# Performance work log

Hardware: AMD Instinct MI355X
Metric: run time of the kernel (lower is better)

Reference implementation:

```python
import jax, jax.numpy as jnp
import numpy as np

NEG_SLOPE = 0.2  # PyG GATConv default leaky_relu slope

def _xavier(key, shape):
    fan_in, fan_out = shape[0], shape[-1]
    lim = float(np.sqrt(6.0 / (fan_in + fan_out)))
    return jax.random.uniform(key, shape, jnp.float32, -lim, lim)

def setup_inputs() -> dict:
    key = jax.random.key(0)
    ks = jax.random.split(key, 12)
    B, N, F_in, Hd, H = 32768, 12, 128, 64, 4
    return {
        'node_features': jax.random.normal(ks[0], (B, N, F_in), jnp.float32),
        # GAT layer 1: 128 -> 64 per head, 4 heads, concat
        'W1': _xavier(ks[1], (F_in, H * Hd)),
        'att_src1': _xavier(ks[2], (H, Hd)),
        'att_dst1': _xavier(ks[3], (H, Hd)),
        'b1': jnp.zeros((H * Hd,), jnp.float32),
        # GAT layer 2: 256 -> 64, 1 head, no concat
        'W2': _xavier(ks[4], (H * Hd, Hd)),
        'att_src2': _xavier(ks[5], (1, Hd)),
        'att_dst2': _xavier(ks[6], (1, Hd)),
        'b2': jnp.zeros((Hd,), jnp.float32),
        # classifier 64 -> 32 -> 1
        'Wc1': _xavier(ks[7], (Hd, Hd // 2)),
        'bc1': jnp.zeros((Hd // 2,), jnp.float32),
        'Wc2': _xavier(ks[8], (Hd // 2, 1)),
        'bc2': jnp.zeros((1,), jnp.float32),
    }

def gat_layer(x, W, a_src, a_dst, b, concat):
    # x: [B, N, Fin]; fully-connected graph with self loops (PyG add_self_loops=True)
    B, N, _ = x.shape
    H, D = a_src.shape
    h = (x @ W).reshape(B, N, H, D)                      # [B,N,H,D]
    es = jnp.einsum('bnhd,hd->bhn', h, a_src)            # source logits per node
    ed = jnp.einsum('bnhd,hd->bhn', h, a_dst)            # dest logits per node
    # logits[b,h,i,j] for edge j->i
    logits = jax.nn.leaky_relu(ed[:, :, :, None] + es[:, :, None, :], NEG_SLOPE)
    alpha = jax.nn.softmax(logits, axis=-1)              # softmax over sources j
    out = jnp.einsum('bhij,bjhd->bihd', alpha, h)        # [B,N,H,D]
    if concat:
        out = out.reshape(B, N, H * D)
    else:
        out = out.mean(axis=2)
    return out + b

def reference(node_features, W1, att_src1, att_dst1, b1, W2, att_src2, att_dst2, b2, Wc1, bc1, Wc2, bc2):
    x = gat_layer(node_features, W1, att_src1, att_dst1, b1, concat=True)
    x = jax.nn.elu(x)
    x = gat_layer(x, W2, att_src2, att_dst2, b2, concat=False)
    x = jax.nn.elu(x)
    g = x.mean(axis=1)                                   # global mean pool over 12 nodes
    hcls = jax.nn.relu(g @ Wc1 + bc1)
    return hcls @ Wc2 + bc2                              # [B, 1]
```

## Files before the change

kernel.cpp:

```cpp
#include <hip/hip_runtime.h>
#include <math.h>


typedef __attribute__((ext_vector_type(8))) short bf16x8;
typedef __attribute__((ext_vector_type(4))) float f32x4;
typedef unsigned short u16;
typedef unsigned int u32;

constexpr int NN  = 12;
constexpr int FIN = 128;
constexpr int C1  = 256;
constexpr int DD  = 64;
#define NEG 0.2f

constexpr int WS_W1H = 0, WS_W1L = 32768, WS_W2H = 65536, WS_W2L = 81920;

__device__ __forceinline__ u16 f2bf(float f) {
    u32 u = __float_as_uint(f);
    u += 0x7fffu + ((u >> 16) & 1u);
    return (u16)(u >> 16);
}
__device__ __forceinline__ float bf2f(u16 h) { return __uint_as_float(((u32)h) << 16); }
__device__ __forceinline__ float bflo(u32 u) { return __uint_as_float(u << 16); }
__device__ __forceinline__ float bfhi(u32 u) { return __uint_as_float(u & 0xffff0000u); }

__global__ void prep_weights(const float* __restrict__ W1,
                             const float* __restrict__ W2,
                             u16* __restrict__ ws) {
    int idx = blockIdx.x * 256 + threadIdx.x;
    if (idx < 32768) {
        int j = idx & 7, lane = (idx >> 3) & 63, ks = (idx >> 9) & 3, nt = idx >> 11;
        int k = ks * 32 + (lane >> 4) * 8 + j;
        int c = nt * 16 + (lane & 15);
        float v = W1[k * C1 + c];
        u16 hi = f2bf(v);
        ws[WS_W1H + idx] = hi;
        ws[WS_W1L + idx] = f2bf(v - bf2f(hi));
    } else if (idx < 49152) {
        int i2 = idx - 32768;
        int j = i2 & 7, lane = (i2 >> 3) & 63, ks = (i2 >> 9) & 7, nt = i2 >> 12;
        int k = ks * 32 + (lane >> 4) * 8 + j;
        int c = nt * 16 + (lane & 15);
        float v = W2[k * DD + c];
        u16 hi = f2bf(v);
        ws[WS_W2H + i2] = hi;
        ws[WS_W2L + i2] = f2bf(v - bf2f(hi));
    }
}

__global__ __launch_bounds__(256, 3) void gat_fused(
    const float* __restrict__ x_in,
    const u16*  __restrict__ wtab,
    const float* __restrict__ asrc1, const float* __restrict__ adst1,
    const float* __restrict__ b1,
    const float* __restrict__ asrc2, const float* __restrict__ adst2,
    const float* __restrict__ b2,
    const float* __restrict__ Wc1,  const float* __restrict__ bc1,
    const float* __restrict__ Wc2,  const float* __restrict__ bc2,
    float* __restrict__ out)
{
    __shared__ __align__(16) unsigned char s_union[34816];
    u16* s_xh  = (u16*)s_union;
    u16* s_xl  = s_xh + 32 * 136;
    u16* s_h1h = (u16*)s_union;
    u16* s_h1l = s_h1h + 32 * 264;
    __shared__ __align__(16) float s_alpha[2][4][NN][NN];
    __shared__ float s_es[2][4][NN], s_ed[2][4][NN];
    __shared__ __align__(16) float s_alpha2[2][NN][NN];
    __shared__ float s_es2[2][NN], s_ed2[2][NN];
    __shared__ __align__(16) float s_h2[24 * DD];
    __shared__ float s_gmean[2][DD];
    __shared__ float s_hc[2][32];

    const int t = threadIdx.x;
    const int lane = t & 63, wave = t >> 6;
    const long b0 = (long)blockIdx.x * 2;

    {
        const float4* src = (const float4*)(x_in + b0 * NN * FIN);
        #pragma unroll
        for (int j = 0; j < 3; ++j) {
            int p = j * 256 + t;
            float4 v = src[p];
            int row = p >> 5, col = (p & 31) * 4;
            ushort4 h, l;
            h.x = f2bf(v.x); l.x = f2bf(v.x - bf2f(h.x));
            h.y = f2bf(v.y); l.y = f2bf(v.y - bf2f(h.y));
            h.z = f2bf(v.z); l.z = f2bf(v.z - bf2f(h.z));
            h.w = f2bf(v.w); l.w = f2bf(v.w - bf2f(h.w));
            *(ushort4*)&s_xh[row * 136 + col] = h;
            *(ushort4*)&s_xl[row * 136 + col] = l;
        }
        for (int i = t; i < 544; i += 256) {
            ((u32*)(s_xh + 24 * 136))[i] = 0u;
            ((u32*)(s_xl + 24 * 136))[i] = 0u;
        }
    }
    __syncthreads();

    {
        const int arow = lane & 15, aks = lane >> 4;
        bf16x8 ah[2][4], al[2][4];
        #pragma unroll
        for (int m = 0; m < 2; ++m)
            #pragma unroll
            for (int ks = 0; ks < 4; ++ks) {
                int off = (m * 16 + arow) * 136 + ks * 32 + aks * 8;
                ah[m][ks] = *(const bf16x8*)&s_xh[off];
                al[m][ks] = *(const bf16x8*)&s_xl[off];
            }
        __syncthreads();

        #pragma unroll
        for (int nti = 0; nti < 4; ++nti) {
            const int nt = wave * 4 + nti;
            bf16x8 bh[4], bl[4];
            #pragma unroll
            for (int ks = 0; ks < 4; ++ks) {
                int off = ((nt * 4 + ks) * 64 + lane) * 8;
                bh[ks] = *(const bf16x8*)&wtab[WS_W1H + off];
                bl[ks] = *(const bf16x8*)&wtab[WS_W1L + off];
            }
            f32x4 acc[2] = { {0.f,0.f,0.f,0.f}, {0.f,0.f,0.f,0.f} };
            #pragma unroll
            for (int ks = 0; ks < 4; ++ks)
                #pragma unroll
                for (int m = 0; m < 2; ++m) {
                    acc[m] = __builtin_amdgcn_mfma_f32_16x16x32_bf16(ah[m][ks], bh[ks], acc[m], 0, 0, 0);
                    acc[m] = __builtin_amdgcn_mfma_f32_16x16x32_bf16(ah[m][ks], bl[ks], acc[m], 0, 0, 0);
                    acc[m] = __builtin_amdgcn_mfma_f32_16x16x32_bf16(al[m][ks], bh[ks], acc[m], 0, 0, 0);
                    acc[m] = __builtin_amdgcn_mfma_f32_16x16x32_bf16(al[m][ks], bl[ks], acc[m], 0, 0, 0);
                }
            const int ccol = nt * 16 + (lane & 15);
            #pragma unroll
            for (int m = 0; m < 2; ++m)
                #pragma unroll
                for (int r = 0; r < 4; ++r) {
                    int row = m * 16 + (lane >> 4) * 4 + r;
                    float v = acc[m][r];
                    u16 hi = f2bf(v);
                    s_h1h[row * 264 + ccol] = hi;
                    s_h1l[row * 264 + ccol] = f2bf(v - bf2f(hi));
                }
        }
    }
    __syncthreads();

    if (t < 192) {
        int tmp = t;
        const int n = tmp % NN; tmp /= NN;
        const int h = tmp & 3; tmp >>= 2;
        const int sflag = tmp & 1;
        const int g = tmp >> 1;
        const float* att = (sflag ? adst1 : asrc1) + h * DD;
        const int base = (g * NN + n) * 264 + h * DD;
        float sum = 0.f;
        #pragma unroll
        for (int it = 0; it < 8; ++it) {
            const int ch = ((it + t) & 7) * 8;
            uint4 uh = *(const uint4*)&s_h1h[base + ch];
            uint4 ul = *(const uint4*)&s_h1l[base + ch];
            float4 a0 = *(const float4*)&att[ch];
            float4 a1 = *(const float4*)&att[ch + 4];
            sum += (bflo(uh.x) + bflo(ul.x)) * a0.x;
            sum += (bfhi(uh.x) + bfhi(ul.x)) * a0.y;
            sum += (bflo(uh.y) + bflo(ul.y)) * a0.z;
            sum += (bfhi(uh.y) + bfhi(ul.y)) * a0.w;
            sum += (bflo(uh.z) + bflo(ul.z)) * a1.x;
            sum += (bfhi(uh.z) + bfhi(ul.z)) * a1.y;
            sum += (bflo(uh.w) + bflo(ul.w)) * a1.z;
            sum += (bfhi(uh.w) + bfhi(ul.w)) * a1.w;
        }
        if (sflag) s_ed[g][h][n] = sum; else s_es[g][h][n] = sum;
    }
    __syncthreads();

    if (t < 96) {
        const int i = t % NN;
        const int h = (t / NN) & 3;
        const int g = t / (NN * 4);
        const float edv = s_ed[g][h][i];
        float l[NN];
        float m = -3.4e38f;
        #pragma unroll
        for (int j = 0; j < NN; ++j) {
            float v = edv + s_es[g][h][j];
            v = (v >= 0.f) ? v : NEG * v;
            l[j] = v; m = fmaxf(m, v);
        }
        float s = 0.f;
        #pragma unroll
        for (int j = 0; j < NN; ++j) { float p = __expf(l[j] - m); l[j] = p; s += p; }
        const float inv = 1.f / s;
        #pragma unroll
        for (int j = 0; j < NN; ++j) s_alpha[g][h][i][j] = l[j] * inv;
    }
    __syncthreads();

    {
        const int c = t;
        const int hh = c >> 6;
        const float bias = b1[c];
        #pragma unroll
        for (int g = 0; g < 2; ++g) {
            float hcol[NN];
            #pragma unroll
            for (int j = 0; j < NN; ++j) {
                int off = (g * NN + j) * 264 + c;
                hcol[j] = bf2f(s_h1h[off]) + bf2f(s_h1l[off]);
            }
            float x2v[NN];
            #pragma unroll
            for (int i = 0; i < NN; ++i) {
                const float4* ar = (const float4*)&s_alpha[g][hh][i][0];
                float4 q0 = ar[0], q1 = ar[1], q2 = ar[2];
                float o = q0.x*hcol[0] + q0.y*hcol[1] + q0.z*hcol[2] + q0.w*hcol[3]
                        + q1.x*hcol[4] + q1.y*hcol[5] + q1.z*hcol[6] + q1.w*hcol[7]
                        + q2.x*hcol[8] + q2.y*hcol[9] + q2.z*hcol[10] + q2.w*hcol[11];
                o += bias;
                x2v[i] = (o > 0.f) ? o : (__expf(o) - 1.f);
            }
            #pragma unroll
            for (int i = 0; i < NN; ++i) {
                int off = (g * NN + i) * 264 + c;
                u16 hi = f2bf(x2v[i]);
                s_h1h[off] = hi;
                s_h1l[off] = f2bf(x2v[i] - bf2f(hi));
            }
        }
    }
    __syncthreads();

    {
        const int arow = lane & 15, aks = lane >> 4;
        f32x4 acc[2] = { {0.f,0.f,0.f,0.f}, {0.f,0.f,0.f,0.f} };
        #pragma unroll
        for (int ks = 0; ks < 8; ++ks) {
            int woff = ((wave * 8 + ks) * 64 + lane) * 8;
            bf16x8 bh = *(const bf16x8*)&wtab[WS_W2H + woff];
            bf16x8 bl = *(const bf16x8*)&wtab[WS_W2L + woff];
            #pragma unroll
            for (int m = 0; m < 2; ++m) {
                int off = (m * 16 + arow) * 264 + ks * 32 + aks * 8;
                bf16x8 ah = *(const bf16x8*)&s_h1h[off];
                bf16x8 al = *(const bf16x8*)&s_h1l[off];
                acc[m] = __builtin_amdgcn_mfma_f32_16x16x32_bf16(ah, bh, acc[m], 0, 0, 0);
                acc[m] = __builtin_amdgcn_mfma_f32_16x16x32_bf16(ah, bl, acc[m], 0, 0, 0);
                acc[m] = __builtin_amdgcn_mfma_f32_16x16x32_bf16(al, bh, acc[m], 0, 0, 0);
                acc[m] = __builtin_amdgcn_mfma_f32_16x16x32_bf16(al, bl, acc[m], 0, 0, 0);
            }
        }
        const int ccol = wave * 16 + (lane & 15);
        #pragma unroll
        for (int m = 0; m < 2; ++m)
            #pragma unroll
            for (int r = 0; r < 4; ++r) {
                int row = m * 16 + (lane >> 4) * 4 + r;
                if (row < 24) s_h2[row * DD + ccol] = acc[m][r];
            }
    }
    __syncthreads();

    if (t < 48) {
        const int n = t % NN;
        const int sflag = (t / NN) & 1;
        const int g = t / (NN * 2);
        const float* att = sflag ? adst2 : asrc2;
        const float* row = s_h2 + (g * NN + n) * DD;
        float sum = 0.f;
        #pragma unroll
        for (int it = 0; it < 16; ++it) {
            const int dch = ((it + t) & 15) * 4;
            float4 hv = *(const float4*)&row[dch];
            float4 av = *(const float4*)&att[dch];
            sum += hv.x * av.x + hv.y * av.y + hv.z * av.z + hv.w * av.w;
        }
        if (sflag) s_ed2[g][n] = sum; else s_es2[g][n] = sum;
    }
    __syncthreads();
    if (t < 24) {
        const int i = t % NN;
        const int g = t / NN;
        const float edv = s_ed2[g][i];
        float l[NN];
        float m = -3.4e38f;
        #pragma unroll
        for (int j = 0; j < NN; ++j) {
            float v = edv + s_es2[g][j];
            v = (v >= 0.f) ? v : NEG * v;
            l[j] = v; m = fmaxf(m, v);
        }
        float s = 0.f;
        #pragma unroll
        for (int j = 0; j < NN; ++j) { float p = __expf(l[j] - m); l[j] = p; s += p; }
        const float inv = 1.f / s;
        #pragma unroll
        for (int j = 0; j < NN; ++j) s_alpha2[g][i][j] = l[j] * inv;
    }
    __syncthreads();

    if (t < 128) {
        const int g = t >> 6;
        const int d = t & 63;
        float hcol[NN];
        #pragma unroll
        for (int j = 0; j < NN; ++j) hcol[j] = s_h2[(g * NN + j) * DD + d];
        const float bias = b2[d];
        float gsum = 0.f;
        #pragma unroll
        for (int i = 0; i < NN; ++i) {
            const float4* ar = (const float4*)&s_alpha2[g][i][0];
            float4 q0 = ar[0], q1 = ar[1], q2 = ar[2];
            float o = q0.x*hcol[0] + q0.y*hcol[1] + q0.z*hcol[2] + q0.w*hcol[3]
                    + q1.x*hcol[4] + q1.y*hcol[5] + q1.z*hcol[6] + q1.w*hcol[7]
                    + q2.x*hcol[8] + q2.y*hcol[9] + q2.z*hcol[10] + q2.w*hcol[11];
            o += bias;
            o = (o > 0.f) ? o : (__expf(o) - 1.f);
            gsum += o;
        }
        s_gmean[g][d] = gsum * (1.f / 12.f);
    }
    __syncthreads();

    if (t < 64) {
        const int g = t >> 5;
        const int m = t & 31;
        float sum = bc1[m];
        #pragma unroll
        for (int d = 0; d < DD; ++d) sum = fmaf(s_gmean[g][d], Wc1[d * 32 + m], sum);
        s_hc[g][m] = (sum > 0.f) ? sum : 0.f;
    }
    __syncthreads();
    if (t < 2) {
        float sum = bc2[0];
        #pragma unroll
        for (int m = 0; m < 32; ++m) sum = fmaf(s_hc[t][m], Wc2[m], sum);
        out[b0 + t] = sum;
    }
}

extern "C" void kernel_launch(void* const* d_in, const int* in_sizes, int n_in,
                              void* d_out, int out_size, void* d_ws, size_t ws_size,
                              hipStream_t stream) {
    const float* x     = (const float*)d_in[0];
    const float* W1    = (const float*)d_in[1];
    const float* asrc1 = (const float*)d_in[2];
    const float* adst1 = (const float*)d_in[3];
    const float* b1    = (const float*)d_in[4];
    const float* W2    = (const float*)d_in[5];
    const float* asrc2 = (const float*)d_in[6];
    const float* adst2 = (const float*)d_in[7];
    const float* b2    = (const float*)d_in[8];
    const float* Wc1   = (const float*)d_in[9];
    const float* bc1   = (const float*)d_in[10];
    const float* Wc2   = (const float*)d_in[11];
    const float* bc2   = (const float*)d_in[12];
    float* outp = (float*)d_out;

    const int B = in_sizes[0] / (NN * FIN);
    u16* wtab = (u16*)d_ws;

    hipLaunchKernelGGL(prep_weights, dim3(192), dim3(256), 0, stream, W1, W2, wtab);
    hipLaunchKernelGGL(gat_fused, dim3(B / 2), dim3(256), 0, stream,
                       x, wtab, asrc1, adst1, b1, asrc2, adst2, b2,
                       Wc1, bc1, Wc2, bc2, outp);
}
```

Baseline: 628.8 us.

## Swizzle MFMA operand layout, keep h1 in fp32, drop lo*lo MFMA term

Stores the split-bf16 A operands (x and the layer-2 input) in LDS using an XOR-swizzled, fragment-major layout so each lane reads one contiguous 16-byte chunk without bank conflicts. The layer-1 output h1 is now kept as fp32 in padded LDS rows instead of being split into hi/lo bf16 halves, which removes the conversion and decode work. The lo*lo MFMA term is dropped in both GEMMs, removing a quarter of the matrix instructions at a small accuracy cost. The s_h2 rows are padded to 68 to reduce bank conflicts, and an extra barrier is added so the layer-2 input can reuse the h1 buffer.

```diff
diff --git a/kernel.cpp b/kernel.cpp
--- a/kernel.cpp
+++ b/kernel.cpp
@@ -21,8 +21,7 @@
     return (u16)(u >> 16);
 }
 __device__ __forceinline__ float bf2f(u16 h) { return __uint_as_float(((u32)h) << 16); }
-__device__ __forceinline__ float bflo(u32 u) { return __uint_as_float(u << 16); }
-__device__ __forceinline__ float bfhi(u32 u) { return __uint_as_float(u & 0xffff0000u); }
+__device__ __forceinline__ int swz(int u) { return u ^ ((u >> 4) & 7); }
 
 __global__ void prep_weights(const float* __restrict__ W1,
                              const float* __restrict__ W2,
@@ -59,16 +58,17 @@
     const float* __restrict__ Wc2,  const float* __restrict__ bc2,
     float* __restrict__ out)
 {
-    __shared__ __align__(16) unsigned char s_union[34816];
-    u16* s_xh  = (u16*)s_union;
-    u16* s_xl  = s_xh + 32 * 136;
-    u16* s_h1h = (u16*)s_union;
-    u16* s_h1l = s_h1h + 32 * 264;
+    __shared__ __align__(16) unsigned char s_union[32768];
+    u16*   s_xfh  = (u16*)s_union;
+    u16*   s_xfl  = (u16*)(s_union + 8192);
+    float* s_h1f  = (float*)s_union;
+    u16*   s_x2h  = (u16*)s_union;
+    u16*   s_x2l  = (u16*)(s_union + 16384);
     __shared__ __align__(16) float s_alpha[2][4][NN][NN];
     __shared__ float s_es[2][4][NN], s_ed[2][4][NN];
     __shared__ __align__(16) float s_alpha2[2][NN][NN];
     __shared__ float s_es2[2][NN], s_ed2[2][NN];
-    __shared__ __align__(16) float s_h2[24 * DD];
+    __shared__ __align__(16) float s_h2[24 * 68];
     __shared__ float s_gmean[2][DD];
     __shared__ float s_hc[2][32];
 
@@ -82,32 +82,36 @@
         for (int j = 0; j < 3; ++j) {
             int p = j * 256 + t;
             float4 v = src[p];
-            int row = p >> 5, col = (p & 31) * 4;
+            int row = p >> 5, cb = (p & 31) * 4;
+            int m = row >> 4, r15 = row & 15;
+            int ks = cb >> 5, aks = (cb >> 3) & 3, jj = cb & 7;
+            int us = swz((ks * 2 + m) * 64 + aks * 16 + r15);
             ushort4 h, l;
             h.x = f2bf(v.x); l.x = f2bf(v.x - bf2f(h.x));
             h.y = f2bf(v.y); l.y = f2bf(v.y - bf2f(h.y));
             h.z = f2bf(v.z); l.z = f2bf(v.z - bf2f(h.z));
             h.w = f2bf(v.w); l.w = f2bf(v.w - bf2f(h.w));
-            *(ushort4*)&s_xh[row * 136 + col] = h;
-            *(ushort4*)&s_xl[row * 136 + col] = l;
-        }
-        for (int i = t; i < 544; i += 256) {
-            ((u32*)(s_xh + 24 * 136))[i] = 0u;
-            ((u32*)(s_xl + 24 * 136))[i] = 0u;
+            *(ushort4*)&s_xfh[us * 8 + jj] = h;
+            *(ushort4*)&s_xfl[us * 8 + jj] = l;
+        }
+        if (t < 128) {
+            int ks = t >> 5, aks = (t >> 3) & 3, r15 = 8 + (t & 7);
+            int us = swz((ks * 2 + 1) * 64 + aks * 16 + r15);
+            *(uint4*)&s_xfh[us * 8] = make_uint4(0, 0, 0, 0);
+            *(uint4*)&s_xfl[us * 8] = make_uint4(0, 0, 0, 0);
         }
     }
     __syncthreads();
 
     {
-        const int arow = lane & 15, aks = lane >> 4;
         bf16x8 ah[2][4], al[2][4];
         #pragma unroll
         for (int m = 0; m < 2; ++m)
             #pragma unroll
             for (int ks = 0; ks < 4; ++ks) {
-                int off = (m * 16 + arow) * 136 + ks * 32 + aks * 8;
-                ah[m][ks] = *(const bf16x8*)&s_xh[off];
-                al[m][ks] = *(const bf16x8*)&s_xl[off];
+                int us = swz((ks * 2 + m) * 64 + lane);
+                ah[m][ks] = *(const bf16x8*)&s_xfh[us * 8];
+                al[m][ks] = *(const bf16x8*)&s_xfl[us * 8];
             }
         __syncthreads();
 
@@ -129,7 +133,6 @@
                     acc[m] = __builtin_amdgcn_mfma_f32_16x16x32_bf16(ah[m][ks], bh[ks], acc[m], 0, 0, 0);
                     acc[m] = __builtin_amdgcn_mfma_f32_16x16x32_bf16(ah[m][ks], bl[ks], acc[m], 0, 0, 0);
                     acc[m] = __builtin_amdgcn_mfma_f32_16x16x32_bf16(al[m][ks], bh[ks], acc[m], 0, 0, 0);
-                    acc[m] = __builtin_amdgcn_mfma_f32_16x16x32_bf16(al[m][ks], bl[ks], acc[m], 0, 0, 0);
                 }
             const int ccol = nt * 16 + (lane & 15);
             #pragma unroll
@@ -137,10 +140,7 @@
                 #pragma unroll
                 for (int r = 0; r < 4; ++r) {
                     int row = m * 16 + (lane >> 4) * 4 + r;
-                    float v = acc[m][r];
-                    u16 hi = f2bf(v);
-                    s_h1h[row * 264 + ccol] = hi;
-                    s_h1l[row * 264 + ccol] = f2bf(v - bf2f(hi));
+                    if (row < 24) s_h1f[row * 268 + ccol] = acc[m][r];
                 }
         }
     }
@@ -153,23 +153,17 @@
         const int sflag = tmp & 1;
         const int g = tmp >> 1;
         const float* att = (sflag ? adst1 : asrc1) + h * DD;
-        const int base = (g * NN + n) * 264 + h * DD;
+        const float* row = s_h1f + (g * NN + n) * 268 + h * DD;
         float sum = 0.f;
         #pragma unroll
         for (int it = 0; it < 8; ++it) {
             const int ch = ((it + t) & 7) * 8;
-            uint4 uh = *(const uint4*)&s_h1h[base + ch];
-            uint4 ul = *(const uint4*)&s_h1l[base + ch];
+            float4 h0 = *(const float4*)&row[ch];
+            float4 h1v = *(const float4*)&row[ch + 4];
             float4 a0 = *(const float4*)&att[ch];
             float4 a1 = *(const float4*)&att[ch + 4];
-            sum += (bflo(uh.x) + bflo(ul.x)) * a0.x;
-            sum += (bfhi(uh.x) + bfhi(ul.x)) * a0.y;
-            sum += (bflo(uh.y) + bflo(ul.y)) * a0.z;
-            sum += (bfhi(uh.y) + bfhi(ul.y)) * a0.w;
-            sum += (bflo(uh.z) + bflo(ul.z)) * a1.x;
-            sum += (bfhi(uh.z) + bfhi(ul.z)) * a1.y;
-            sum += (bflo(uh.w) + bflo(ul.w)) * a1.z;
-            sum += (bfhi(uh.w) + bfhi(ul.w)) * a1.w;
+            sum += h0.x*a0.x + h0.y*a0.y + h0.z*a0.z + h0.w*a0.w
+                 + h1v.x*a1.x + h1v.y*a1.y + h1v.z*a1.z + h1v.w*a1.w;
         }
         if (sflag) s_ed[g][h][n] = sum; else s_es[g][h][n] = sum;
     }
@@ -201,15 +195,12 @@
         const int c = t;
         const int hh = c >> 6;
         const float bias = b1[c];
+        float x2v[2][NN];
         #pragma unroll
         for (int g = 0; g < 2; ++g) {
             float hcol[NN];
             #pragma unroll
-            for (int j = 0; j < NN; ++j) {
-                int off = (g * NN + j) * 264 + c;
-                hcol[j] = bf2f(s_h1h[off]) + bf2f(s_h1l[off]);
-            }
-            float x2v[NN];
+            for (int j = 0; j < NN; ++j) hcol[j] = s_h1f[(g * NN + j) * 268 + c];
             #pragma unroll
             for (int i = 0; i < NN; ++i) {
                 const float4* ar = (const float4*)&s_alpha[g][hh][i][0];
@@ -218,21 +209,33 @@
                         + q1.x*hcol[4] + q1.y*hcol[5] + q1.z*hcol[6] + q1.w*hcol[7]
                         + q2.x*hcol[8] + q2.y*hcol[9] + q2.z*hcol[10] + q2.w*hcol[11];
                 o += bias;
-                x2v[i] = (o > 0.f) ? o : (__expf(o) - 1.f);
-            }
+                x2v[g][i] = (o > 0.f) ? o : (__expf(o) - 1.f);
+            }
+        }
+        __syncthreads();
+
+        const int ks_c = c >> 5, aks_c = (c >> 3) & 3, j_c = c & 7;
+        #pragma unroll
+        for (int g = 0; g < 2; ++g)
             #pragma unroll
             for (int i = 0; i < NN; ++i) {
-                int off = (g * NN + i) * 264 + c;
-                u16 hi = f2bf(x2v[i]);
-                s_h1h[off] = hi;
-                s_h1l[off] = f2bf(x2v[i] - bf2f(hi));
-            }
+                int row = g * NN + i;
+                int us = swz((ks_c * 2 + (row >> 4)) * 64 + aks_c * 16 + (row & 15));
+                float v = x2v[g][i];
+                u16 hi = f2bf(v);
+                s_x2h[us * 8 + j_c] = hi;
+                s_x2l[us * 8 + j_c] = f2bf(v - bf2f(hi));
+            }
+        {
+            int ks = t >> 5, aks = (t >> 3) & 3, r15 = 8 + (t & 7);
+            int us = swz((ks * 2 + 1) * 64 + aks * 16 + r15);
+            *(uint4*)&s_x2h[us * 8] = make_uint4(0, 0, 0, 0);
+            *(uint4*)&s_x2l[us * 8] = make_uint4(0, 0, 0, 0);
         }
     }
     __syncthreads();
 
     {
-        const int arow = lane & 15, aks = lane >> 4;
         f32x4 acc[2] = { {0.f,0.f,0.f,0.f}, {0.f,0.f,0.f,0.f} };
         #pragma unroll
         for (int ks = 0; ks < 8; ++ks) {
@@ -241,13 +244,12 @@
             bf16x8 bl = *(const bf16x8*)&wtab[WS_W2L + woff];
             #pragma unroll
             for (int m = 0; m < 2; ++m) {
-                int off = (m * 16 + arow) * 264 + ks * 32 + aks * 8;
-                bf16x8 ah = *(const bf16x8*)&s_h1h[off];
-                bf16x8 al = *(const bf16x8*)&s_h1l[off];
+                int us = swz((ks * 2 + m) * 64 + lane);
+                bf16x8 ah = *(const bf16x8*)&s_x2h[us * 8];
+                bf16x8 al = *(const bf16x8*)&s_x2l[us * 8];
                 acc[m] = __builtin_amdgcn_mfma_f32_16x16x32_bf16(ah, bh, acc[m], 0, 0, 0);
                 acc[m] = __builtin_amdgcn_mfma_f32_16x16x32_bf16(ah, bl, acc[m], 0, 0, 0);
                 acc[m] = __builtin_amdgcn_mfma_f32_16x16x32_bf16(al, bh, acc[m], 0, 0, 0);
-                acc[m] = __builtin_amdgcn_mfma_f32_16x16x32_bf16(al, bl, acc[m], 0, 0, 0);
             }
         }
         const int ccol = wave * 16 + (lane & 15);
@@ -256,7 +258,7 @@
             #pragma unroll
             for (int r = 0; r < 4; ++r) {
                 int row = m * 16 + (lane >> 4) * 4 + r;
-                if (row < 24) s_h2[row * DD + ccol] = acc[m][r];
+                if (row < 24) s_h2[row * 68 + ccol] = acc[m][r];
             }
     }
     __syncthreads();
@@ -266,7 +268,7 @@
         const int sflag = (t / NN) & 1;
         const int g = t / (NN * 2);
         const float* att = sflag ? adst2 : asrc2;
-        const float* row = s_h2 + (g * NN + n) * DD;
+        const float* row = s_h2 + (g * NN + n) * 68;
         float sum = 0.f;
         #pragma unroll
         for (int it = 0; it < 16; ++it) {
@@ -304,7 +306,7 @@
         const int d = t & 63;
         float hcol[NN];
         #pragma unroll
-        for (int j = 0; j < NN; ++j) hcol[j] = s_h2[(g * NN + j) * DD + d];
+        for (int j = 0; j < NN; ++j) hcol[j] = s_h2[(g * NN + j) * 68 + d];
         const float bias = b2[d];
         float gsum = 0.f;
         #pragma unroll
```

Result: faster. 559.7 us (-11.0%).
